# Performance work log

Hardware: AMD Instinct MI355X
Metric: run time of the kernel (lower is better)

The kernel has to match this reference:

```python
import jax, jax.numpy as jnp
import numpy as np

N_NODES = 50000
N_EDGES = 800000
D_IN = 128
D_HID = 128
D_OUT = 128


def setup_inputs() -> dict:
    key = jax.random.key(0)
    ks = jax.random.split(key, 5)
    x = jax.random.normal(ks[0], (N_NODES, D_IN), dtype=jnp.float32)
    edge_index = jax.random.randint(ks[1], (2, N_EDGES), 0, N_NODES, dtype=jnp.int64)
    # Glorot-ish init for the two GCN linear weights (PyG uses glorot)
    W1 = jax.random.normal(ks[2], (D_IN, D_HID), dtype=jnp.float32) * (1.0 / np.sqrt(D_IN))
    b1 = jnp.zeros((D_HID,), dtype=jnp.float32)
    W2 = jax.random.normal(ks[3], (D_HID, D_OUT), dtype=jnp.float32) * (1.0 / np.sqrt(D_HID))
    b2 = jnp.zeros((D_OUT,), dtype=jnp.float32)
    return {"x": x, "edge_index": edge_index, "W1": W1, "b1": b1, "W2": W2, "b2": b2}


def _gcn_layer(x, W, b, src, dst, dinv):
    """PyG GCNConv: h = xW; out[j] = sum_{(i->j)} dinv[i]*dinv[j]*h[i] + dinv[j]^2*h[j] (self-loop) + b."""
    n = x.shape[0]
    h = x @ W                                   # [N, D_out]
    coef = (dinv[src] * dinv[dst])[:, None]     # [E, 1] symmetric norm
    msg = h[src] * coef                         # [E, D_out] gather + scale
    agg = jax.ops.segment_sum(msg, dst, num_segments=n)  # scatter-add
    agg = agg + h * (dinv * dinv)[:, None]      # self-loop contribution
    return agg + b


def reference(x, edge_index, W1, b1, W2, b2):
    src = edge_index[0]
    dst = edge_index[1]
    n = x.shape[0]
    # degree over target nodes, including the added self-loop (+1)
    deg = jax.ops.segment_sum(jnp.ones_like(dst, dtype=x.dtype), dst, num_segments=n) + 1.0
    dinv = jax.lax.rsqrt(deg)
    h = jax.nn.relu(_gcn_layer(x, W1, b1, src, dst, dinv))
    return _gcn_layer(h, W2, b2, src, dst, dinv)
```

## Files before the change

### kernel.cpp

```cpp
#include <hip/hip_runtime.h>
#include <hip/hip_fp16.h>

#define NN 50000
#define NE 800000
#define D 128
#define NBLK ((NN + 255) / 256)

typedef __attribute__((ext_vector_type(8))) _Float16 f16x8;
typedef __attribute__((ext_vector_type(8))) short short8;
typedef __attribute__((ext_vector_type(4))) float f32x4;

__global__ __launch_bounds__(256) void k_count(const int* __restrict__ dst, int* __restrict__ cnt,
                                               int* __restrict__ rank) {
    int e = blockIdx.x * 256 + threadIdx.x;
    if (e < NE) rank[e] = atomicAdd(&cnt[dst[e]], 1);
}

__global__ __launch_bounds__(256) void k_scan_partial(const int* __restrict__ cnt, int* __restrict__ blockSums) {
    __shared__ int s[256];
    int t = threadIdx.x;
    int i = blockIdx.x * 256 + t;
    s[t] = (i < NN) ? cnt[i] : 0;
    __syncthreads();
    for (int off = 128; off > 0; off >>= 1) {
        if (t < off) s[t] += s[t + off];
        __syncthreads();
    }
    if (t == 0) blockSums[blockIdx.x] = s[0];
}

__global__ __launch_bounds__(256) void k_scan_blocks(int* __restrict__ blockSums, int* __restrict__ row_ptr) {
    __shared__ int s[256];
    int t = threadIdx.x;
    int v = (t < NBLK) ? blockSums[t] : 0;
    s[t] = v;
    __syncthreads();
    for (int off = 1; off < 256; off <<= 1) {
        int y = (t >= off) ? s[t - off] : 0;
        __syncthreads();
        s[t] += y;
        __syncthreads();
    }
    if (t < NBLK) blockSums[t] = s[t] - v;
    if (t == 0) row_ptr[NN] = NE;
}

__global__ __launch_bounds__(256) void k_scan_final(const int* __restrict__ cnt, const int* __restrict__ blockOffs,
                                                    int* __restrict__ row_ptr, float* __restrict__ dinv) {
    __shared__ int s[256];
    int t = threadIdx.x;
    int i = blockIdx.x * 256 + t;
    int v = (i < NN) ? cnt[i] : 0;
    s[t] = v;
    __syncthreads();
    for (int off = 1; off < 256; off <<= 1) {
        int y = (t >= off) ? s[t - off] : 0;
        __syncthreads();
        s[t] += y;
        __syncthreads();
    }
    if (i < NN) {
        row_ptr[i] = s[t] - v + blockOffs[blockIdx.x];
        dinv[i] = rsqrtf((float)v + 1.0f);
    }
}

__global__ __launch_bounds__(256) void k_fill(const int* __restrict__ src, const int* __restrict__ dst,
                                              const int* __restrict__ rank, const int* __restrict__ row_ptr,
                                              unsigned short* __restrict__ csr) {
    int e = blockIdx.x * 256 + threadIdx.x;
    if (e < NE) {
        int d = dst[e];
        csr[row_ptr[d] + rank[e]] = (unsigned short)src[e];
    }
}

__global__ __launch_bounds__(256) void k_prepw(const float* __restrict__ W1, const float* __restrict__ W2,
                                               char* __restrict__ img1, char* __restrict__ img2) {
    int b = blockIdx.x;
    const float* W = (b < 64) ? W1 : W2;
    char* img = (b < 64) ? img1 : img2;
    int e = (b & 63) * 256 + threadIdx.x;
    int k = e >> 7, n = e & 127;
    float f = W[e];
    __half hi = __float2half_rn(f);
    float rem = f - __half2float(hi);
    __half lo = __float2half_rn(rem);
    unsigned off = (unsigned)((n << 8) + (k << 1)) ^ (unsigned)((n & 7) << 4);
    *(__half*)(img + off) = hi;
    *(__half*)(img + 32768 + off) = lo;
}

template <bool RELU_IN, bool A_FP16>
__global__ __launch_bounds__(256) void k_mgemm(const void* __restrict__ Av, const char* __restrict__ wimg,
                                               __half* __restrict__ H) {
    __shared__ char lds[65536];
    const int t = threadIdx.x;

    {
        const float4* gv = (const float4*)wimg;
        float4* lv = (float4*)lds;
#pragma unroll
        for (int i = 0; i < 16; ++i) lv[i * 256 + t] = gv[i * 256 + t];
    }
    __syncthreads();

    const int lane = t & 63;
    const int wv = t >> 6;
    const int r0 = blockIdx.x * 64 + wv * 16;
    const int rl = lane & 15;
    const int g = lane >> 4;
    int arow = r0 + rl;
    if (arow >= NN) arow = NN - 1;

    f32x4 acc[8];
#pragma unroll
    for (int j = 0; j < 8; ++j) acc[j] = (f32x4){0.f, 0.f, 0.f, 0.f};

#pragma unroll
    for (int ks = 0; ks < 4; ++ks) {
        f16x8 a;
        if (A_FP16) {
            const __half* A = (const __half*)Av;
            float4 raw = *(const float4*)(A + (size_t)arow * D + ks * 32 + g * 8);
            if (RELU_IN) {
                short8 s = __builtin_bit_cast(short8, raw);
#pragma unroll
                for (int i = 0; i < 8; ++i) s[i] = (s[i] & (short)0x8000) ? (short)0 : s[i];
                a = __builtin_bit_cast(f16x8, s);
            } else {
                a = __builtin_bit_cast(f16x8, raw);
            }
        } else {
            const float* A = (const float*)Av;
            const float* ar = A + (size_t)arow * D + ks * 32 + g * 8;
            float4 p0 = *(const float4*)ar;
            float4 p1 = *(const float4*)(ar + 4);
            float av8[8] = {p0.x, p0.y, p0.z, p0.w, p1.x, p1.y, p1.z, p1.w};
#pragma unroll
            for (int i = 0; i < 8; ++i) {
                float f = RELU_IN ? fmaxf(av8[i], 0.f) : av8[i];
                a[i] = (_Float16)f;
            }
        }
        const int kofs = (ks * 32 + g * 8) << 1;
#pragma unroll
        for (int j = 0; j < 8; ++j) {
            int n = j * 16 + rl;
            unsigned off = (unsigned)((n << 8) + kofs) ^ (unsigned)((n & 7) << 4);
            f16x8 bh = *(const f16x8*)(lds + off);
            f16x8 bl = *(const f16x8*)(lds + 32768 + off);
            acc[j] = __builtin_amdgcn_mfma_f32_16x16x32_f16(a, bh, acc[j], 0, 0, 0);
            acc[j] = __builtin_amdgcn_mfma_f32_16x16x32_f16(a, bl, acc[j], 0, 0, 0);
        }
    }

#pragma unroll
    for (int j = 0; j < 8; ++j) {
#pragma unroll
        for (int i = 0; i < 4; ++i) {
            int row = r0 + g * 4 + i;
            if (row < NN) H[(size_t)row * D + j * 16 + rl] = __float2half(acc[j][i]);
        }
    }
}

template <bool OUT_FP16>
__global__ __launch_bounds__(256) void k_pull(const __half* __restrict__ H, const float* __restrict__ dinv,
                                              const float* __restrict__ b, const int* __restrict__ row_ptr,
                                              const unsigned short* __restrict__ csr, void* __restrict__ outv) {
    int wid = (blockIdx.x * 256 + threadIdx.x) >> 6;
    int lane = threadIdx.x & 63;
    int node = __builtin_amdgcn_readfirstlane(wid);
    int rl = lane & 15;
    int g = lane >> 4;

    float dd = dinv[node];

    float2 a0 = {0.f, 0.f}, a1 = {0.f, 0.f}, a2 = {0.f, 0.f}, a3 = {0.f, 0.f};
    float2 c0b = {0.f, 0.f}, c1b = {0.f, 0.f}, c2b = {0.f, 0.f}, c3b = {0.f, 0.f};

    int beg = row_ptr[node];
    int end = row_ptr[node + 1];
    for (int i = beg + g; i < end; i += 8) {
        int i1 = i + 4;
        bool ok = i1 < end;
        int s0 = csr[i];
        int s1 = csr[ok ? i1 : i];
        float c0 = dinv[s0] * dd;
        float c1 = ok ? dinv[s1] * dd : 0.f;
        float4 raw0 = *(const float4*)(H + (size_t)s0 * D + rl * 8);
        float4 raw1 = *(const float4*)(H + (size_t)s1 * D + rl * 8);
        const __half2* h0 = (const __half2*)&raw0;
        const __half2* h1 = (const __half2*)&raw1;
        float2 f0 = __half22float2(h0[0]);
        float2 f1 = __half22float2(h0[1]);
        float2 f2 = __half22float2(h0[2]);
        float2 f3 = __half22float2(h0[3]);
        a0.x = fmaf(f0.x, c0, a0.x); a0.y = fmaf(f0.y, c0, a0.y);
        a1.x = fmaf(f1.x, c0, a1.x); a1.y = fmaf(f1.y, c0, a1.y);
        a2.x = fmaf(f2.x, c0, a2.x); a2.y = fmaf(f2.y, c0, a2.y);
        a3.x = fmaf(f3.x, c0, a3.x); a3.y = fmaf(f3.y, c0, a3.y);
        float2 g0 = __half22float2(h1[0]);
        float2 g1 = __half22float2(h1[1]);
        float2 g2 = __half22float2(h1[2]);
        float2 g3 = __half22float2(h1[3]);
        c0b.x = fmaf(g0.x, c1, c0b.x); c0b.y = fmaf(g0.y, c1, c0b.y);
        c1b.x = fmaf(g1.x, c1, c1b.x); c1b.y = fmaf(g1.y, c1, c1b.y);
        c2b.x = fmaf(g2.x, c1, c2b.x); c2b.y = fmaf(g2.y, c1, c2b.y);
        c3b.x = fmaf(g3.x, c1, c3b.x); c3b.y = fmaf(g3.y, c1, c3b.y);
    }
    a0.x += c0b.x; a0.y += c0b.y;
    a1.x += c1b.x; a1.y += c1b.y;
    a2.x += c2b.x; a2.y += c2b.y;
    a3.x += c3b.x; a3.y += c3b.y;

    float v[8] = {a0.x, a0.y, a1.x, a1.y, a2.x, a2.y, a3.x, a3.y};
#pragma unroll
    for (int i = 0; i < 8; ++i) {
        v[i] += __shfl_xor(v[i], 16);
        v[i] += __shfl_xor(v[i], 32);
    }

    if (g == 0) {
        float s2 = dd * dd;
        float4 raw = *(const float4*)(H + (size_t)node * D + rl * 8);
        const __half2* hh = (const __half2*)&raw;
        float2 s0 = __half22float2(hh[0]);
        float2 s1 = __half22float2(hh[1]);
        float2 s2v = __half22float2(hh[2]);
        float2 s3 = __half22float2(hh[3]);
        float4 b0 = ((const float4*)b)[rl * 2];
        float4 b1v = ((const float4*)b)[rl * 2 + 1];
        float r[8];
        r[0] = fmaf(s0.x, s2, v[0] + b0.x);
        r[1] = fmaf(s0.y, s2, v[1] + b0.y);
        r[2] = fmaf(s1.x, s2, v[2] + b0.z);
        r[3] = fmaf(s1.y, s2, v[3] + b0.w);
        r[4] = fmaf(s2v.x, s2, v[4] + b1v.x);
        r[5] = fmaf(s2v.y, s2, v[5] + b1v.y);
        r[6] = fmaf(s3.x, s2, v[6] + b1v.z);
        r[7] = fmaf(s3.y, s2, v[7] + b1v.w);
        if (OUT_FP16) {
            __half* out = (__half*)outv;
            __half2 o[4];
            o[0] = __floats2half2_rn(r[0], r[1]);
            o[1] = __floats2half2_rn(r[2], r[3]);
            o[2] = __floats2half2_rn(r[4], r[5]);
            o[3] = __floats2half2_rn(r[6], r[7]);
            *(float4*)(out + (size_t)node * D + rl * 8) = *(float4*)o;
        } else {
            float* out = (float*)outv;
            float* op = out + (size_t)node * D + rl * 8;
            *(float4*)op = make_float4(r[0], r[1], r[2], r[3]);
            *(float4*)(op + 4) = make_float4(r[4], r[5], r[6], r[7]);
        }
    }
}

extern "C" void kernel_launch(void* const* d_in, const int* in_sizes, int n_in,
                              void* d_out, int out_size, void* d_ws, size_t ws_size,
                              hipStream_t stream) {
    const float* x  = (const float*)d_in[0];
    const int*   ei = (const int*)d_in[1];
    const float* W1 = (const float*)d_in[2];
    const float* b1 = (const float*)d_in[3];
    const float* W2 = (const float*)d_in[4];
    const float* b2 = (const float*)d_in[5];
    float* out = (float*)d_out;

    const int* src = ei;
    const int* dst = ei + NE;

    char* ws = (char*)d_ws;
    int*    cnt       = (int*)   (ws + 0);
    int*    row_ptr   = (int*)   (ws + 204800);
    int*    blockSums = (int*)   (ws + 409600);
    float*  dinv      = (float*) (ws + 410624);
    char*   wimg1     = (char*)  (ws + 614400);
    char*   wimg2     = (char*)  (ws + 679936);
    int*    rank      = (int*)   (ws + 745472);
    unsigned short* csr = (unsigned short*)(ws + 3945472);
    __half* h         = (__half*)(ws + 5545472);
    __half* h2        = (__half*)(ws + 18345472);

    const int nBlkEdge = (NE + 255) / 256;
    const int nBlkGemm = (NN + 63) / 64;
    const int nBlkPull = NN / 4;

    hipMemsetAsync(cnt, 0, (size_t)NN * 4, stream);
    k_count<<<nBlkEdge, 256, 0, stream>>>(dst, cnt, rank);
    k_scan_partial<<<NBLK, 256, 0, stream>>>(cnt, blockSums);
    k_scan_blocks<<<1, 256, 0, stream>>>(blockSums, row_ptr);
    k_scan_final<<<NBLK, 256, 0, stream>>>(cnt, blockSums, row_ptr, dinv);
    k_fill<<<nBlkEdge, 256, 0, stream>>>(src, dst, rank, row_ptr, csr);
    k_prepw<<<128, 256, 0, stream>>>(W1, W2, wimg1, wimg2);

    k_mgemm<false, false><<<nBlkGemm, 256, 0, stream>>>(x, wimg1, h);
    k_pull<true><<<nBlkPull, 256, 0, stream>>>(h, dinv, b1, row_ptr, csr, h2);

    k_mgemm<true, true><<<nBlkGemm, 256, 0, stream>>>(h2, wimg2, h);
    k_pull<false><<<nBlkPull, 256, 0, stream>>>(h, dinv, b2, row_ptr, csr, out);
}
```

Baseline: 234.1 us.

## Merge preprocessing kernels to cut launches and shrink rank array to u16

Folds the memset and weight-image preparation into one init kernel. It also merges the block-offset scan into the final scan, with each block reducing the partial sums before it, and runs the CSR fill and the first GEMM as one launch split by block index. The rank array is stored as 16-bit values to halve its traffic. This removes several kernel launches and their serialization gaps. The cost is redundant per-block reduction work, and the fill and GEMM blocks now share one kernel that reserves 64KB LDS even for the fill blocks, which may limit occupancy.

```diff
diff --git a/kernel.cpp b/kernel.cpp
--- a/kernel.cpp
+++ b/kernel.cpp
@@ -5,15 +5,39 @@
 #define NE 800000
 #define D 128
 #define NBLK ((NN + 255) / 256)
+#define NBLK_GEMM ((NN + 63) / 64)
 
 typedef __attribute__((ext_vector_type(8))) _Float16 f16x8;
 typedef __attribute__((ext_vector_type(8))) short short8;
 typedef __attribute__((ext_vector_type(4))) float f32x4;
 
+__global__ __launch_bounds__(256) void k_init(int* __restrict__ cnt,
+                                              const float* __restrict__ W1, const float* __restrict__ W2,
+                                              char* __restrict__ img1, char* __restrict__ img2) {
+    int b = blockIdx.x;
+    if (b < NBLK) {
+        int i = b * 256 + threadIdx.x;
+        if (i < NN) cnt[i] = 0;
+    } else {
+        int pb = b - NBLK;
+        const float* W = (pb < 64) ? W1 : W2;
+        char* img = (pb < 64) ? img1 : img2;
+        int e = (pb & 63) * 256 + threadIdx.x;
+        int k = e >> 7, n = e & 127;
+        float f = W[e];
+        __half hi = __float2half_rn(f);
+        float rem = f - __half2float(hi);
+        __half lo = __float2half_rn(rem);
+        unsigned off = (unsigned)((n << 8) + (k << 1)) ^ (unsigned)((n & 7) << 4);
+        *(__half*)(img + off) = hi;
+        *(__half*)(img + 32768 + off) = lo;
+    }
+}
+
 __global__ __launch_bounds__(256) void k_count(const int* __restrict__ dst, int* __restrict__ cnt,
-                                               int* __restrict__ rank) {
+                                               unsigned short* __restrict__ rank) {
     int e = blockIdx.x * 256 + threadIdx.x;
-    if (e < NE) rank[e] = atomicAdd(&cnt[dst[e]], 1);
+    if (e < NE) rank[e] = (unsigned short)atomicAdd(&cnt[dst[e]], 1);
 }
 
 __global__ __launch_bounds__(256) void k_scan_partial(const int* __restrict__ cnt, int* __restrict__ blockSums) {
@@ -29,10 +53,22 @@
     if (t == 0) blockSums[blockIdx.x] = s[0];
 }
 
-__global__ __launch_bounds__(256) void k_scan_blocks(int* __restrict__ blockSums, int* __restrict__ row_ptr) {
+__global__ __launch_bounds__(256) void k_scan_final(const int* __restrict__ cnt, const int* __restrict__ blockSums,
+                                                    int* __restrict__ row_ptr, float* __restrict__ dinv) {
     __shared__ int s[256];
     int t = threadIdx.x;
-    int v = (t < NBLK) ? blockSums[t] : 0;
+
+    s[t] = (t < NBLK && t < (int)blockIdx.x) ? blockSums[t] : 0;
+    __syncthreads();
+    for (int off = 128; off > 0; off >>= 1) {
+        if (t < off) s[t] += s[t + off];
+        __syncthreads();
+    }
+    int blockOff = s[0];
+    __syncthreads();
+
+    int i = blockIdx.x * 256 + t;
+    int v = (i < NN) ? cnt[i] : 0;
     s[t] = v;
     __syncthreads();
     for (int off = 1; off < 256; off <<= 1) {
@@ -41,62 +77,17 @@
         s[t] += y;
         __syncthreads();
     }
-    if (t < NBLK) blockSums[t] = s[t] - v;
-    if (t == 0) row_ptr[NN] = NE;
-}
-
-__global__ __launch_bounds__(256) void k_scan_final(const int* __restrict__ cnt, const int* __restrict__ blockOffs,
-                                                    int* __restrict__ row_ptr, float* __restrict__ dinv) {
-    __shared__ int s[256];
-    int t = threadIdx.x;
-    int i = blockIdx.x * 256 + t;
-    int v = (i < NN) ? cnt[i] : 0;
-    s[t] = v;
-    __syncthreads();
-    for (int off = 1; off < 256; off <<= 1) {
-        int y = (t >= off) ? s[t - off] : 0;
-        __syncthreads();
-        s[t] += y;
-        __syncthreads();
-    }
     if (i < NN) {
-        row_ptr[i] = s[t] - v + blockOffs[blockIdx.x];
+        row_ptr[i] = s[t] - v + blockOff;
         dinv[i] = rsqrtf((float)v + 1.0f);
     }
-}
-
-__global__ __launch_bounds__(256) void k_fill(const int* __restrict__ src, const int* __restrict__ dst,
-                                              const int* __restrict__ rank, const int* __restrict__ row_ptr,
-                                              unsigned short* __restrict__ csr) {
-    int e = blockIdx.x * 256 + threadIdx.x;
-    if (e < NE) {
-        int d = dst[e];
-        csr[row_ptr[d] + rank[e]] = (unsigned short)src[e];
-    }
-}
-
-__global__ __launch_bounds__(256) void k_prepw(const float* __restrict__ W1, const float* __restrict__ W2,
-                                               char* __restrict__ img1, char* __restrict__ img2) {
-    int b = blockIdx.x;
-    const float* W = (b < 64) ? W1 : W2;
-    char* img = (b < 64) ? img1 : img2;
-    int e = (b & 63) * 256 + threadIdx.x;
-    int k = e >> 7, n = e & 127;
-    float f = W[e];
-    __half hi = __float2half_rn(f);
-    float rem = f - __half2float(hi);
-    __half lo = __float2half_rn(rem);
-    unsigned off = (unsigned)((n << 8) + (k << 1)) ^ (unsigned)((n & 7) << 4);
-    *(__half*)(img + off) = hi;
-    *(__half*)(img + 32768 + off) = lo;
+    if (blockIdx.x == 0 && t == 0) row_ptr[NN] = NE;
 }
 
 template <bool RELU_IN, bool A_FP16>
-__global__ __launch_bounds__(256) void k_mgemm(const void* __restrict__ Av, const char* __restrict__ wimg,
-                                               __half* __restrict__ H) {
-    __shared__ char lds[65536];
-    const int t = threadIdx.x;
-
+static __device__ __forceinline__ void gemm_core(char* lds, const void* __restrict__ Av,
+                                                 const char* __restrict__ wimg, __half* __restrict__ H,
+                                                 int bid, int t) {
     {
         const float4* gv = (const float4*)wimg;
         float4* lv = (float4*)lds;
@@ -107,7 +98,7 @@
 
     const int lane = t & 63;
     const int wv = t >> 6;
-    const int r0 = blockIdx.x * 64 + wv * 16;
+    const int r0 = bid * 64 + wv * 16;
     const int rl = lane & 15;
     const int g = lane >> 4;
     int arow = r0 + rl;
@@ -163,6 +154,32 @@
             if (row < NN) H[(size_t)row * D + j * 16 + rl] = __float2half(acc[j][i]);
         }
     }
+}
+
+__global__ __launch_bounds__(256) void k_fill_gemm1(const int* __restrict__ src, const int* __restrict__ dst,
+                                                    const unsigned short* __restrict__ rank,
+                                                    const int* __restrict__ row_ptr,
+                                                    unsigned short* __restrict__ csr,
+                                                    const float* __restrict__ x, const char* __restrict__ wimg,
+                                                    __half* __restrict__ H) {
+    __shared__ char lds[65536];
+    int bid = blockIdx.x;
+    if (bid < NBLK_GEMM) {
+        gemm_core<false, false>(lds, x, wimg, H, bid, threadIdx.x);
+    } else {
+        int e = (bid - NBLK_GEMM) * 256 + threadIdx.x;
+        if (e < NE) {
+            int d = dst[e];
+            csr[row_ptr[d] + rank[e]] = (unsigned short)src[e];
+        }
+    }
+}
+
+template <bool RELU_IN, bool A_FP16>
+__global__ __launch_bounds__(256) void k_mgemm(const void* __restrict__ Av, const char* __restrict__ wimg,
+                                               __half* __restrict__ H) {
+    __shared__ char lds[65536];
+    gemm_core<RELU_IN, A_FP16>(lds, Av, wimg, H, blockIdx.x, threadIdx.x);
 }
 
 template <bool OUT_FP16>
@@ -279,26 +296,20 @@
     float*  dinv      = (float*) (ws + 410624);
     char*   wimg1     = (char*)  (ws + 614400);
     char*   wimg2     = (char*)  (ws + 679936);
-    int*    rank      = (int*)   (ws + 745472);
-    unsigned short* csr = (unsigned short*)(ws + 3945472);
-    __half* h         = (__half*)(ws + 5545472);
-    __half* h2        = (__half*)(ws + 18345472);
+    unsigned short* rank = (unsigned short*)(ws + 745472);
+    unsigned short* csr  = (unsigned short*)(ws + 2345472);
+    __half* h         = (__half*)(ws + 3945472);
+    __half* h2        = (__half*)(ws + 16745472);
 
     const int nBlkEdge = (NE + 255) / 256;
-    const int nBlkGemm = (NN + 63) / 64;
     const int nBlkPull = NN / 4;
 
-    hipMemsetAsync(cnt, 0, (size_t)NN * 4, stream);
+    k_init<<<NBLK + 128, 256, 0, stream>>>(cnt, W1, W2, wimg1, wimg2);
     k_count<<<nBlkEdge, 256, 0, stream>>>(dst, cnt, rank);
     k_scan_partial<<<NBLK, 256, 0, stream>>>(cnt, blockSums);
-    k_scan_blocks<<<1, 256, 0, stream>>>(blockSums, row_ptr);
     k_scan_final<<<NBLK, 256, 0, stream>>>(cnt, blockSums, row_ptr, dinv);
-    k_fill<<<nBlkEdge, 256, 0, stream>>>(src, dst, rank, row_ptr, csr);
-    k_prepw<<<128, 256, 0, stream>>>(W1, W2, wimg1, wimg2);
-
-    k_mgemm<false, false><<<nBlkGemm, 256, 0, stream>>>(x, wimg1, h);
+    k_fill_gemm1<<<NBLK_GEMM + nBlkEdge, 256, 0, stream>>>(src, dst, rank, row_ptr, csr, x, wimg1, h);
     k_pull<true><<<nBlkPull, 256, 0, stream>>>(h, dinv, b1, row_ptr, csr, h2);
-
-    k_mgemm<true, true><<<nBlkGemm, 256, 0, stream>>>(h2, wimg2, h);
+    k_mgemm<true, true><<<NBLK_GEMM, 256, 0, stream>>>(h2, wimg2, h);
     k_pull<false><<<nBlkPull, 256, 0, stream>>>(h, dinv, b2, row_ptr, csr, out);
 }
```

New measurement: 227.5 us. -2.9%, faster.
